# Optimization experiments

Hardware: AMD Instinct MI355X
Metric: run time of the kernel (lower is better)

Reference implementation:

```python
import jax, jax.numpy as jnp
import numpy as np

D_MODEL = 1024
N_HEADS = 16
K_TOP = 64
D_HEAD = D_MODEL // N_HEADS


def setup_inputs() -> dict:
    key = jax.random.key(0)
    ks = jax.random.split(key, 9)
    B, L = 8, 4096
    bound = 1.0 / np.sqrt(D_MODEL)  # nn.Linear default init range
    lin = lambda k: jax.random.uniform(k, (D_MODEL, D_MODEL), jnp.float32, -bound, bound)
    vec = lambda k: jax.random.uniform(k, (D_MODEL,), jnp.float32, -bound, bound)
    return {
        "query": jax.random.normal(ks[0], (B, L, D_MODEL), jnp.float32),
        "Wq": lin(ks[1]), "bq": vec(ks[2]),
        "Wk": lin(ks[3]), "bk": vec(ks[4]),
        "Wv": lin(ks[5]), "bv": vec(ks[6]),
        "Wo": lin(ks[7]), "bo": vec(ks[8]),
    }


def reference(query, Wq, bq, Wk, bk, Wv, bv, Wo, bo):
    B, L_q, D = query.shape
    L_k = L_q  # self-attention: key = value = query
    F_q = L_q // 2 + 1
    F_k = L_k // 2 + 1
    k_top = min(K_TOP, F_q)

    def proj(x, W, b):
        # (B, L, D) -> (B, H, L, d_head)
        return (x @ W + b).reshape(B, -1, N_HEADS, D_HEAD).transpose(0, 2, 1, 3)

    q = proj(query, Wq, bq)
    k = proj(query, Wk, bk)
    v = proj(query, Wv, bv)

    q_freq = jnp.fft.rfft(q, axis=2)  # (B, H, F_q, d_head) complex64
    k_freq = jnp.fft.rfft(k, axis=2)
    v_freq = jnp.fft.rfft(v, axis=2)

    # top-k frequency bins by mean spectral magnitude of the query
    q_energy = jnp.abs(q_freq).mean(axis=-1)  # (B, H, F_q)
    _, idx = jax.lax.top_k(q_energy, k_top)   # (B, H, k)
    mapped_idx = jnp.clip(
        jnp.round(idx.astype(jnp.float32) * (F_k - 1) / (F_q - 1)).astype(jnp.int32),
        0, F_k - 1)

    gather = lambda x, i: jnp.take_along_axis(x, i[..., None], axis=2)
    q_top = gather(q_freq, idx)          # (B, H, k, d_head)
    k_top_freq = gather(k_freq, mapped_idx)
    v_top = gather(v_freq, mapped_idx)

    eps = 1e-8
    attn_score = (q_top.real * k_top_freq.real).sum(-1) / (D_HEAD ** 0.5 + eps)
    attn = jax.nn.softmax(attn_score, axis=-1)[..., None]  # (B, H, k, 1)

    # fill spectrum with mean of query spectrum, then scatter attended bins
    q_mean_freq = q_freq.mean(axis=2, keepdims=True)  # (B, H, 1, d_head) complex
    out_freq = jnp.broadcast_to(q_mean_freq, (B, N_HEADS, F_q, D_HEAD))
    src = (attn * v_top.real).astype(out_freq.dtype)  # real -> complex (imag=0)
    bi = jnp.arange(B)[:, None, None]
    hi = jnp.arange(N_HEADS)[None, :, None]
    out_freq = out_freq.at[bi, hi, idx].set(src)

    out_time = jnp.fft.irfft(out_freq, n=L_q, axis=2)  # (B, H, L, d_head)
    out = out_time.transpose(0, 2, 1, 3).reshape(B, L_q, D)
    return out @ Wo + bo
```

## Files before the change

### kernel.cpp

```cpp
#include <hip/hip_runtime.h>
#include <math.h>
#include <stdint.h>


typedef _Float16 f16;
typedef _Float16 f16x4 __attribute__((ext_vector_type(4)));
typedef _Float16 f16x8 __attribute__((ext_vector_type(8)));
typedef float f32x4 __attribute__((ext_vector_type(4)));

#define PI_F 3.14159265358979323846f
#define PADJ(j) ((j) + ((j) >> 3))

__device__ __forceinline__ void gl_lds16(const void* g, void* l) {
  __builtin_amdgcn_global_load_lds((const __attribute__((address_space(1))) void*)g,
                                   (__attribute__((address_space(3))) void*)l, 16, 0, 0);
}

__device__ __forceinline__ float2 cadd(float2 a, float2 b) { return make_float2(a.x + b.x, a.y + b.y); }
__device__ __forceinline__ float2 csub(float2 a, float2 b) { return make_float2(a.x - b.x, a.y - b.y); }
__device__ __forceinline__ float2 cmul(float2 a, float2 b) {
  return make_float2(a.x * b.x - a.y * b.y, a.x * b.y + a.y * b.x);
}
__device__ __forceinline__ float2 cmni(float2 a) { return make_float2(a.y, -a.x); }

template <int NIT>
__device__ __forceinline__ void stgP(const char* g, size_t gstride, int kb, char* lds,
                                     int tid, int w) {
#pragma unroll
  for (int it = 0; it < NIT; ++it) {
    int ls = it * 256 + tid;
    int j = ls >> 3, s = ls & 7;
    int u = s ^ (j & 7);
    int grow = 2 * j + (u >> 2);
    gl_lds16(g + (size_t)grow * gstride + ((u & 3) << 4) + kb, lds + it * 4096 + w * 1024);
  }
}

__device__ __forceinline__ int pofs(int grow, int q) {
  int j = grow >> 1;
  int u = ((grow & 1) << 2) | q;
  return j * 128 + ((u ^ (j & 7)) << 4);
}

__global__ __launch_bounds__(256) void k_tw(float2* __restrict__ twtab, float2* __restrict__ utab) {
  int j = blockIdx.x * 256 + threadIdx.x;
  if (j < 2048) {
    float ang = (float)j * (-6.28318530717958647692f / 2048.0f);
    twtab[j] = make_float2(cosf(ang), sinf(ang));
  } else if (j < 4097) {
    int f = j - 2048;
    float ang = (float)f * (-6.28318530717958647692f / 4096.0f);
    utab[f] = make_float2(cosf(ang), sinf(ang));
  }
}

__global__ __launch_bounds__(256) void k_prep(const float* __restrict__ Wq, const float* __restrict__ Wo,
                                              f16* __restrict__ WqT, f16* __restrict__ WoT) {
  __shared__ float t[32][33];
  const float* src = blockIdx.z ? Wo : Wq;
  f16* dst = blockIdx.z ? WoT : WqT;
  int c0 = blockIdx.x * 32, r0 = blockIdx.y * 32;
  int tx = threadIdx.x, ty = threadIdx.y;
#pragma unroll
  for (int yy = 0; yy < 4; ++yy)
    t[ty + yy * 8][tx] = src[(size_t)(r0 + ty + yy * 8) * 1024 + c0 + tx];
  __syncthreads();
#pragma unroll
  for (int yy = 0; yy < 4; ++yy)
    dst[(size_t)(c0 + ty + yy * 8) * 1024 + r0 + tx] = (f16)t[tx][ty + yy * 8];
}

__global__ __launch_bounds__(256) void k_prep2(const float* __restrict__ Wk, const float* __restrict__ Wv,
                                               f16* __restrict__ WkT, f16* __restrict__ WvT) {
  __shared__ float t[32][33];
  const float* src = blockIdx.z ? Wv : Wk;
  f16* dst = blockIdx.z ? WvT : WkT;
  int c0 = blockIdx.x * 32, r0 = blockIdx.y * 32;
  int tx = threadIdx.x, ty = threadIdx.y;
#pragma unroll
  for (int yy = 0; yy < 4; ++yy)
    t[ty + yy * 8][tx] = src[(size_t)(r0 + ty + yy * 8) * 1024 + c0 + tx];
  __syncthreads();
#pragma unroll
  for (int yy = 0; yy < 4; ++yy)
    dst[(size_t)(c0 + ty + yy * 8) * 1024 + r0 + tx] = (f16)t[tx][ty + yy * 8];
}

__global__ __launch_bounds__(256) void k_t1(const float* __restrict__ X, f16* __restrict__ Xt16) {
  __shared__ float t[64][65];
  int b = blockIdx.z;
  int l0 = blockIdx.x * 64, d0 = blockIdx.y * 64;
  int tid = threadIdx.x;
#pragma unroll
  for (int it = 0; it < 16; ++it) {
    int lr = it * 4 + (tid >> 6);
    t[lr][tid & 63] = X[((size_t)b * 4096 + l0 + lr) * 1024 + d0 + (tid & 63)];
  }
  __syncthreads();
#pragma unroll
  for (int it = 0; it < 4; ++it) {
    int dd = it * 16 + (tid >> 4);
    int lc = (tid & 15) * 4;
    f16x4 v;
    v[0] = (f16)t[lc][dd]; v[1] = (f16)t[lc + 1][dd];
    v[2] = (f16)t[lc + 2][dd]; v[3] = (f16)t[lc + 3][dd];
    *(f16x4*)&Xt16[((size_t)b * 1024 + d0 + dd) * 4096 + l0 + lc] = v;
  }
}

__device__ __forceinline__ void r8_stage(const float2* __restrict__ cur, float2* __restrict__ nxt,
                                         const float2* __restrict__ tw, int tid, int lg) {
  int Ls = 1 << lg;
  int p = tid >> lg, q = tid & (Ls - 1);
  float2 x[8];
#pragma unroll
  for (int u = 0; u < 8; ++u) x[u] = cur[PADJ(tid + 256 * u)];
  float2 s0 = cadd(x[0], x[4]), d0v = csub(x[0], x[4]);
  float2 s1 = cadd(x[2], x[6]), d1v = csub(x[2], x[6]);
  float2 e0 = cadd(s0, s1), e2 = csub(s0, s1);
  float2 md1 = cmni(d1v);
  float2 e1 = cadd(d0v, md1), e3 = csub(d0v, md1);
  float2 t0 = cadd(x[1], x[5]), u0 = csub(x[1], x[5]);
  float2 t1 = cadd(x[3], x[7]), u1 = csub(x[3], x[7]);
  float2 o0 = cadd(t0, t1), o2 = csub(t0, t1);
  float2 mu1 = cmni(u1);
  float2 o1 = cadd(u0, mu1), o3 = csub(u0, mu1);
  const float C8 = 0.70710678118654752440f;
  float2 w1 = make_float2(C8 * (o1.x + o1.y), C8 * (o1.y - o1.x));
  float2 w2 = cmni(o2);
  float2 w3 = make_float2(C8 * (o3.y - o3.x), -C8 * (o3.x + o3.y));
  float2 y[8];
  y[0] = cadd(e0, o0); y[4] = csub(e0, o0);
  y[1] = cadd(e1, w1); y[5] = csub(e1, w1);
  y[2] = cadd(e2, w2); y[6] = csub(e2, w2);
  y[3] = cadd(e3, w3); y[7] = csub(e3, w3);
  int tb = p << lg;
#pragma unroll
  for (int v = 1; v < 8; ++v) y[v] = cmul(y[v], tw[tb * v]);
  int ob = q + (p << (lg + 3));
#pragma unroll
  for (int v = 0; v < 8; ++v) nxt[PADJ(ob + (v << lg))] = y[v];
}

__global__ __launch_bounds__(256) void k_fft(const f16* __restrict__ Xt16,
                                             const float2* __restrict__ twtab,
                                             const float2* __restrict__ utab,
                                             f16* __restrict__ PReU, f16* __restrict__ PImU,
                                             float* __restrict__ sumXf) {
  __shared__ float2 bufA[2304];
  __shared__ float2 bufB[2304];
  __shared__ float redr[256], redi[256];
  int tid = threadIdx.x;
  int blk = blockIdx.x;

  const f16x8* src = (const f16x8*)(Xt16 + (size_t)blk * 4096);
#pragma unroll
  for (int r = 0; r < 2; ++r) {
    int i8 = r * 256 + tid;
    f16x8 v = src[i8];
#pragma unroll
    for (int j = 0; j < 4; ++j)
      bufA[PADJ(4 * i8 + j)] = make_float2((float)v[2 * j], (float)v[2 * j + 1]);
  }
  __syncthreads();
  r8_stage(bufA, bufB, twtab, tid, 0);
  __syncthreads();
  r8_stage(bufB, bufA, twtab, tid, 3);
  __syncthreads();
  r8_stage(bufA, bufB, twtab, tid, 6);
  __syncthreads();
#pragma unroll
  for (int h = 0; h < 2; ++h) {
    int i = (h << 8) + tid;
    float2 a0 = bufB[PADJ(i)], a1 = bufB[PADJ(i + 512)];
    float2 a2 = bufB[PADJ(i + 1024)], a3 = bufB[PADJ(i + 1536)];
    float2 s02 = cadd(a0, a2), d02 = csub(a0, a2);
    float2 s13 = cadd(a1, a3), d13m = cmni(csub(a1, a3));
    bufA[PADJ(i)] = cadd(s02, s13);
    bufA[PADJ(i + 512)] = cadd(d02, d13m);
    bufA[PADJ(i + 1024)] = csub(s02, s13);
    bufA[PADJ(i + 1536)] = csub(d02, d13m);
  }
  __syncthreads();
  float sumr = 0.f, sumi = 0.f;
  size_t obase = (size_t)blk * 2049;
  for (int f = tid; f <= 2048; f += 256) {
    int fz = f & 2047, fm = (2048 - f) & 2047;
    float2 z = bufA[PADJ(fz)], m = bufA[PADJ(fm)];
    float Er = 0.5f * (z.x + m.x), Ei = 0.5f * (z.y - m.y);
    float Or = 0.5f * (z.y + m.y), Oi = -0.5f * (z.x - m.x);
    float2 wv = utab[f];
    float Xr = Er + wv.x * Or - wv.y * Oi;
    float Xi = Ei + wv.x * Oi + wv.y * Or;
    PReU[obase + f] = (f16)Xr;
    PImU[obase + f] = (f16)Xi;
    sumr += Xr; sumi += Xi;
  }
  __syncthreads();
  redr[tid] = sumr; redi[tid] = sumi;
  __syncthreads();
  for (int s = 128; s > 0; s >>= 1) {
    if (tid < s) { redr[tid] += redr[tid + s]; redi[tid] += redi[tid + s]; }
    __syncthreads();
  }
  if (tid == 0) { sumXf[2 * blk] = redr[0]; sumXf[2 * blk + 1] = redi[0]; }
}

__global__ __launch_bounds__(256) void k_C(const float* __restrict__ sumXf, const float* __restrict__ Wq,
                                           const float* __restrict__ bq,
                                           float* __restrict__ Cre, float* __restrict__ Cim) {
  int b = blockIdx.x >> 2;
  int hd = ((blockIdx.x & 3) << 8) + threadIdx.x;
  float accr = 0.f, acci = 0.f;
  for (int dm = 0; dm < 1024; ++dm) {
    float w = Wq[(size_t)dm * 1024 + hd];
    accr += sumXf[2 * (b * 1024 + dm)] * w;
    acci += sumXf[2 * (b * 1024 + dm) + 1] * w;
  }
  Cre[b * 1024 + hd] = (accr + 4096.0f * bq[hd]) * (1.0f / 2049.0f);
  Cim[b * 1024 + hd] = acci * (1.0f / 2049.0f);
}

__global__ __launch_bounds__(256) void k_t2(const f16* __restrict__ PReU, const f16* __restrict__ PImU,
                                            f16* __restrict__ PT) {
  __shared__ f16 t[32][66];
  int z = blockIdx.z;
  int b = z >> 1, pl = z & 1;
  const f16* src = pl ? PImU : PReU;
  int f0 = blockIdx.x * 32, d0 = blockIdx.y * 64;
  int tid = threadIdx.x;
#pragma unroll
  for (int p = 0; p < 8; ++p) {
    int dm = p * 8 + (tid >> 5);
    int ff = f0 + (tid & 31);
    t[tid & 31][dm] = (ff < 2049) ? src[(size_t)(b * 1024 + d0 + dm) * 2049 + ff] : (f16)0.f;
  }
  __syncthreads();
#pragma unroll
  for (int p = 0; p < 2; ++p) {
    int fr = p * 16 + (tid >> 4);
    int dm = (tid & 15) * 4;
    f16x4 v;
    v[0] = t[fr][dm]; v[1] = t[fr][dm + 1]; v[2] = t[fr][dm + 2]; v[3] = t[fr][dm + 3];
    *(f16x4*)&PT[((size_t)b * 4352 + 2 * (f0 + fr) + pl) * 1024 + d0 + dm] = v;
  }
}

__global__ __launch_bounds__(256, 2) void k_energy(const f16* __restrict__ PT, const f16* __restrict__ WqT,
                                                   const float* __restrict__ bq, float* __restrict__ energy) {
  __shared__ __align__(16) char sM[2][24576];
  int tid = threadIdx.x;
  int lane = tid & 63, w = tid >> 6;
  int lin = blockIdx.x;
  int sw = (lin & 7) * 136 + (lin >> 3);
  int bN = sw & 3, Mblk = sw >> 2;
  int wr = w >> 1, wc = w & 1;
  f32x4 acc[4][8];
#pragma unroll
  for (int mf = 0; mf < 4; ++mf)
#pragma unroll
    for (int nf = 0; nf < 8; ++nf) acc[mf][nf] = 0;

  const char* gA0 = (const char*)PT + (size_t)(Mblk * 128) * 2048;
  const char* gB0 = (const char*)WqT + (size_t)(bN * 256) * 2048;
  int r = lane & 15, q = lane >> 4;
  int aofs[4], bofs[8];
#pragma unroll
  for (int mf = 0; mf < 4; ++mf) aofs[mf] = pofs(wr * 64 + mf * 16 + r, q);
#pragma unroll
  for (int nf = 0; nf < 8; ++nf) bofs[nf] = 8192 + pofs(wc * 128 + nf * 16 + r, q);

  char* b0 = &sM[0][0];
  char* b1 = &sM[1][0];
  auto compute = [&](const char* base) {
    f16x8 aF[4], bF[8];
#pragma unroll
    for (int mf = 0; mf < 4; ++mf) aF[mf] = *(const f16x8*)(base + aofs[mf]);
#pragma unroll
    for (int nf = 0; nf < 8; ++nf) bF[nf] = *(const f16x8*)(base + bofs[nf]);
#pragma unroll
    for (int mf = 0; mf < 4; ++mf)
#pragma unroll
      for (int nf = 0; nf < 8; ++nf)
        acc[mf][nf] = __builtin_amdgcn_mfma_f32_16x16x32_f16(aF[mf], bF[nf], acc[mf][nf], 0, 0, 0);
  };

  stgP<2>(gA0, 2048, 0, b0, tid, w);
  stgP<4>(gB0, 2048, 0, b0 + 8192, tid, w);
  for (int t = 0; t < 16; ++t) {
    int kb1 = (2 * t + 1) * 64;
    stgP<2>(gA0, 2048, kb1, b1, tid, w);
    stgP<4>(gB0, 2048, kb1, b1 + 8192, tid, w);
    asm volatile("s_waitcnt vmcnt(6)\ns_barrier" ::: "memory");
    compute(b0);
    asm volatile("s_barrier" ::: "memory");
    if (t < 15) {
      int kb0 = (2 * t + 2) * 64;
      stgP<2>(gA0, 2048, kb0, b0, tid, w);
      stgP<4>(gB0, 2048, kb0, b0 + 8192, tid, w);
      asm volatile("s_waitcnt vmcnt(6)\ns_barrier" ::: "memory");
    } else {
      asm volatile("s_waitcnt vmcnt(0)\ns_barrier" ::: "memory");
    }
    compute(b1);
    asm volatile("s_barrier" ::: "memory");
  }
  int b = Mblk / 34;
  int tIb = Mblk - b * 34;
  int h0 = bN * 4 + wc * 2;
  bool dc0 = (tIb == 0 && wr == 0 && q == 0);
#pragma unroll
  for (int mf = 0; mf < 4; ++mf) {
    float sE0 = 0.f, sO0 = 0.f, sE1 = 0.f, sO1 = 0.f;
#pragma unroll
    for (int nf = 0; nf < 8; ++nf) {
      float re0 = acc[mf][nf][0], im0 = acc[mf][nf][1];
      float re1 = acc[mf][nf][2], im1 = acc[mf][nf][3];
      if (dc0 && mf == 0) re0 += 4096.0f * bq[(h0 + (nf >> 2)) * 64 + (nf & 3) * 16 + r];
      float m0 = sqrtf(re0 * re0 + im0 * im0);
      float m1 = sqrtf(re1 * re1 + im1 * im1);
      if (nf < 4) { sE0 += m0; sO0 += m1; } else { sE1 += m0; sO1 += m1; }
    }
#pragma unroll
    for (int off = 1; off < 16; off <<= 1) {
      sE0 += __shfl_xor(sE0, off);
      sO0 += __shfl_xor(sO0, off);
      sE1 += __shfl_xor(sE1, off);
      sO1 += __shfl_xor(sO1, off);
    }
    if (r == 0) {
      int fp = tIb * 64 + wr * 32 + mf * 8 + (q << 1);
      energy[((size_t)b * 16 + h0) * 2176 + fp] = sE0 * 0.015625f;
      energy[((size_t)b * 16 + h0) * 2176 + fp + 1] = sO0 * 0.015625f;
      energy[((size_t)b * 16 + h0 + 1) * 2176 + fp] = sE1 * 0.015625f;
      energy[((size_t)b * 16 + h0 + 1) * 2176 + fp + 1] = sO1 * 0.015625f;
    }
  }
}

__global__ __launch_bounds__(256) void k_topk(const float* __restrict__ energy, int* __restrict__ idxb) {
  __shared__ float vals[2049];
  __shared__ unsigned long long wbest[4];
  int tid = threadIdx.x, bh = blockIdx.x;
  const float* e = energy + (size_t)bh * 2176;
  for (int i = tid; i < 2049; i += 256) vals[i] = e[i];
  __syncthreads();
  for (int it = 0; it < 64; ++it) {
    unsigned long long best = 0ull;
    for (int f = tid; f < 2049; f += 256) {
      unsigned b32 = __float_as_uint(vals[f]);
      b32 = (b32 & 0x80000000u) ? ~b32 : (b32 | 0x80000000u);
      unsigned long long k = ((unsigned long long)b32 << 12) | (unsigned)(4095 - f);
      best = (k > best) ? k : best;
    }
#pragma unroll
    for (int off = 32; off > 0; off >>= 1) {
      unsigned long long o = __shfl_xor(best, off);
      best = (o > best) ? o : best;
    }
    if ((tid & 63) == 0) wbest[tid >> 6] = best;
    __syncthreads();
    if (tid == 0) {
      unsigned long long b0 = wbest[0] > wbest[1] ? wbest[0] : wbest[1];
      unsigned long long b1 = wbest[2] > wbest[3] ? wbest[2] : wbest[3];
      unsigned long long bb = b0 > b1 ? b0 : b1;
      int f = 4095 - (int)(bb & 4095ull);
      idxb[bh * 64 + it] = f;
      vals[f] = -1.0f;
    }
    __syncthreads();
  }
}

__global__ __launch_bounds__(256) void k_qkv(const f16* __restrict__ PT, const int* __restrict__ idxb,
                                             const f16* __restrict__ WqT, const f16* __restrict__ WkT,
                                             const f16* __restrict__ WvT, float* __restrict__ part) {
  __shared__ __align__(16) f16 sA[64 * 64];
  __shared__ __align__(16) f16 sB[192 * 64];
  __shared__ int fjs[64];
  int tid = threadIdx.x, lane = tid & 63, w = tid >> 6;
  int bh = blockIdx.x, ks = blockIdx.y;
  int b = bh >> 4, h = bh & 15;
  if (tid < 64) fjs[tid] = idxb[bh * 64 + tid];
  __syncthreads();
  f32x4 acc[4][3];
#pragma unroll
  for (int mf = 0; mf < 4; ++mf)
#pragma unroll
    for (int nf = 0; nf < 3; ++nf) acc[mf][nf] = 0;

  int l8 = lane & 7;
  int lr = lane >> 3;
  int swz = (l8 ^ lr) << 4;

  for (int kt = 0; kt < 4; ++kt) {
    int kbyte = ks * 512 + kt * 128;
#pragma unroll
    for (int t = 0; t < 2; ++t) {
      int ia = w * 2 + t;
      int row = ia * 8 + lr;
      const char* src = (const char*)PT + (size_t)(b * 4352 + 2 * fjs[row]) * 2048 + kbyte + swz;
      gl_lds16(src, (char*)sA + ia * 1024);
    }
#pragma unroll
    for (int t = 0; t < 6; ++t) {
      int ib = w * 6 + t;
      int row = ib * 8 + lr;
      const f16* Wt = (row < 64) ? WqT : (row < 128) ? WkT : WvT;
      const char* src = (const char*)Wt + (size_t)(h * 64 + (row & 63)) * 2048 + kbyte + swz;
      gl_lds16(src, (char*)sB + ib * 1024);
    }
    __syncthreads();
#pragma unroll
    for (int kk = 0; kk < 64; kk += 32) {
      int cb = (kk << 1) + ((lane >> 4) << 4);
      int r = lane & 15;
      f16x8 aF[4], bF[3];
#pragma unroll
      for (int mf = 0; mf < 4; ++mf) {
        int row = mf * 16 + r;
        aF[mf] = *(const f16x8*)((const char*)sA + row * 128 + (cb ^ ((row & 7) << 4)));
      }
#pragma unroll
      for (int nf = 0; nf < 3; ++nf) {
        int row = w * 48 + nf * 16 + r;
        bF[nf] = *(const f16x8*)((const char*)sB + row * 128 + (cb ^ ((row & 7) << 4)));
      }
#pragma unroll
      for (int mf = 0; mf < 4; ++mf)
#pragma unroll
        for (int nf = 0; nf < 3; ++nf)
          acc[mf][nf] = __builtin_amdgcn_mfma_f32_16x16x32_f16(aF[mf], bF[nf], acc[mf][nf], 0, 0, 0);
    }
    __syncthreads();
  }
  float* pb = part + (size_t)(ks * 128 + bh) * 12288;
#pragma unroll
  for (int mf = 0; mf < 4; ++mf)
#pragma unroll
    for (int nf = 0; nf < 3; ++nf)
#pragma unroll
      for (int rr = 0; rr < 4; ++rr) {
        int m = mf * 16 + ((lane >> 4) << 2) + rr;
        int n = w * 48 + nf * 16 + (lane & 15);
        pb[m * 192 + n] = acc[mf][nf][rr];
      }
}

__global__ __launch_bounds__(256) void k_attn2(const float* __restrict__ part, const int* __restrict__ idxb,
                                               const float* __restrict__ bq, const float* __restrict__ bk,
                                               const float* __restrict__ bv, const float* __restrict__ Cre,
                                               f16* __restrict__ ampT) {
  __shared__ float sQKV[64][196];
  __shared__ float scores[64], attns[64];
  __shared__ int fjs[64];
  __shared__ int dcrow;
  int tid = threadIdx.x, bh = blockIdx.x;
  int b = bh >> 4, h = bh & 15;
  if (tid == 0) dcrow = -1;
  __syncthreads();
  if (tid < 64) {
    int f = idxb[bh * 64 + tid];
    fjs[tid] = f;
    if (f == 0) dcrow = tid;
  }
  __syncthreads();
  const float4* p0 = (const float4*)(part + (size_t)bh * 12288);
  const size_t s4 = (size_t)128 * 12288 / 4;
#pragma unroll
  for (int it = 0; it < 12; ++it) {
    int e = it * 256 + tid;
    float4 v0 = p0[e], v1 = p0[e + s4], v2 = p0[e + 2 * s4], v3 = p0[e + 3 * s4];
    float4 v;
    v.x = v0.x + v1.x + v2.x + v3.x;
    v.y = v0.y + v1.y + v2.y + v3.y;
    v.z = v0.z + v1.z + v2.z + v3.z;
    v.w = v0.w + v1.w + v2.w + v3.w;
    int m = e / 48, n0 = (e % 48) * 4;
    *(float4*)&sQKV[m][n0] = v;
  }
  __syncthreads();
  if (dcrow >= 0 && tid < 192) {
    const float* bias = (tid < 64) ? bq : (tid < 128) ? bk : bv;
    sQKV[dcrow][tid] += 4096.0f * bias[h * 64 + (tid & 63)];
  }
  __syncthreads();
  {
    int j = tid >> 2, p = tid & 3;
    float s = 0.f;
#pragma unroll
    for (int c = 0; c < 16; ++c) {
      int cc = p * 16 + c;
      s = fmaf(sQKV[j][cc], sQKV[j][64 + cc], s);
    }
    s += __shfl_xor(s, 1);
    s += __shfl_xor(s, 2);
    if (p == 0) scores[j] = s * 0.125f;
  }
  __syncthreads();
  if (tid < 64) {
    float s = scores[tid];
    float m = s;
#pragma unroll
    for (int off = 32; off > 0; off >>= 1) m = fmaxf(m, __shfl_xor(m, off));
    float ev = expf(s - m);
    float sm = ev;
#pragma unroll
    for (int off = 32; off > 0; off >>= 1) sm += __shfl_xor(sm, off);
    attns[tid] = ev / sm;
  }
  __syncthreads();
  {
    int j = tid >> 2, d0 = (tid & 3) * 16;
    float at = attns[j];
    int fj = fjs[j];
    float wj = (fj == 0 || fj == 2048) ? 0.5f : 1.0f;
#pragma unroll
    for (int q4 = 0; q4 < 4; ++q4) {
      float4 c4 = *(const float4*)&Cre[b * 1024 + h * 64 + d0 + q4 * 4];
      float4 vv = *(const float4*)&sQKV[j][128 + d0 + q4 * 4];
      float av0 = wj * (at * vv.x - c4.x);
      float av1 = wj * (at * vv.y - c4.y);
      float av2 = wj * (at * vv.z - c4.z);
      float av3 = wj * (at * vv.w - c4.w);
      f16* o = ampT + (size_t)bh * 4096 + (d0 + q4 * 4) * 64 + j;
      o[0] = (f16)av0; o[64] = (f16)av1; o[128] = (f16)av2; o[192] = (f16)av3;
    }
  }
}

__global__ __launch_bounds__(256) void k_ot(const f16* __restrict__ ampT, const int* __restrict__ idxb,
                                            const float* __restrict__ Cre, const float* __restrict__ Cim,
                                            f16* __restrict__ OT) {
  __shared__ __align__(16) f16 sAmp[64][72];
  __shared__ float gbuf[256];
  __shared__ int fjs[64];
  int tid = threadIdx.x, lane = tid & 63, w = tid >> 6;
  int bh = blockIdx.x >> 4, tch = blockIdx.x & 15;
  int b = bh >> 4, h = bh & 15;
  if (tid < 64) fjs[tid] = idxb[bh * 64 + tid];
  {
    int row = tid >> 2, seg = tid & 3;
    const f16* src = ampT + (size_t)bh * 4096 + row * 64 + seg * 16;
    f16x8 v0 = *(const f16x8*)src;
    f16x8 v1 = *(const f16x8*)(src + 8);
    *(f16x8*)&sAmp[row][seg * 16] = v0;
    *(f16x8*)&sAmp[row][seg * 16 + 8] = v1;
  }
  __syncthreads();
  int r = lane & 15, q = lane >> 4;
  int tbase = tch * 256 + w * 64;
  const float cang = 0.00153398078788564123f;
  f16x8 aF[4][2];
  float ss[4];
#pragma unroll
  for (int mf = 0; mf < 4; ++mf) {
    int t = tbase + mf * 16 + r;
    float s = 0.f;
#pragma unroll
    for (int kk2 = 0; kk2 < 2; ++kk2) {
      f16x8 a;
#pragma unroll
      for (int jj = 0; jj < 8; ++jj) {
        int j = kk2 * 32 + q * 8 + jj;
        int ridx = (fjs[j] * t) & 4095;
        float sn, cs;
        __sincosf((float)ridx * cang, &sn, &cs);
        s += sn;
        a[jj] = (f16)cs;
      }
      aF[mf][kk2] = a;
    }
    ss[mf] = s;
  }
#pragma unroll
  for (int mf = 0; mf < 4; ++mf) {
    ss[mf] += __shfl_xor(ss[mf], 16);
    ss[mf] += __shfl_xor(ss[mf], 32);
  }
  if (q == 0) {
#pragma unroll
    for (int mf = 0; mf < 4; ++mf) {
      int t = tbase + mf * 16 + r;
      float g = ss[mf];
      if (t & 1) {
        int tp = (t <= 2048) ? t : 4096 - t;
        float sg = (t <= 2048) ? 1.f : -1.f;
        float aa = (float)tp * (PI_F / 4096.0f);
        g -= sg * (cosf(aa) / sinf(aa));
      }
      gbuf[w * 64 + mf * 16 + r] = g;
    }
  }
  f16x8 bF[4][2];
#pragma unroll
  for (int nf = 0; nf < 4; ++nf)
#pragma unroll
    for (int kk2 = 0; kk2 < 2; ++kk2)
      bF[nf][kk2] = *(const f16x8*)&sAmp[nf * 16 + r][kk2 * 32 + q * 8];
  f32x4 acc[4][4];
#pragma unroll
  for (int mf = 0; mf < 4; ++mf)
#pragma unroll
    for (int nf = 0; nf < 4; ++nf) acc[mf][nf] = 0;
#pragma unroll
  for (int kk2 = 0; kk2 < 2; ++kk2)
#pragma unroll
    for (int mf = 0; mf < 4; ++mf)
#pragma unroll
      for (int nf = 0; nf < 4; ++nf)
        acc[mf][nf] = __builtin_amdgcn_mfma_f32_16x16x32_f16(aF[mf][kk2], bF[nf][kk2], acc[mf][nf], 0, 0, 0);
  __syncthreads();
  const float s2L = 2.0f / 4096.0f;
#pragma unroll
  for (int nf = 0; nf < 4; ++nf) {
    int d = nf * 16 + r;
    float cim = Cim[b * 1024 + h * 64 + d];
    float cre = Cre[b * 1024 + h * 64 + d];
#pragma unroll
    for (int mf = 0; mf < 4; ++mf) {
#pragma unroll
      for (int rr = 0; rr < 4; ++rr) {
        int ro = mf * 16 + q * 4 + rr;
        int t = tbase + ro;
        float g = gbuf[w * 64 + ro];
        float val = s2L * (acc[mf][nf][rr] + cim * g) + ((t == 0) ? cre : 0.f);
        OT[((size_t)bh * 4096 + t) * 64 + d] = (f16)val;
      }
    }
  }
}

__global__ __launch_bounds__(256, 2) void k_final(const f16* __restrict__ OT, const f16* __restrict__ WoT,
                                                  const float* __restrict__ bo, float* __restrict__ out) {
  __shared__ __align__(16) char sM[2][24576];
  int tid = threadIdx.x, lane = tid & 63, w = tid >> 6;
  int lin = blockIdx.x;
  int sw = (lin & 7) * 128 + (lin >> 3);
  int bN = sw & 3, Mblk = sw >> 2;
  int wr = w >> 1, wc = w & 1;
  f32x4 acc[4][8];
#pragma unroll
  for (int mf = 0; mf < 4; ++mf)
#pragma unroll
    for (int nf = 0; nf < 8; ++nf) acc[mf][nf] = 0;
  int b = Mblk >> 5, t0 = (Mblk & 31) * 128;
  const char* gB0 = (const char*)WoT + (size_t)(bN * 256) * 2048;
  int r = lane & 15, q = lane >> 4;
  int aofs[4], bofs[8];
#pragma unroll
  for (int mf = 0; mf < 4; ++mf) aofs[mf] = pofs(wr * 64 + mf * 16 + r, q);
#pragma unroll
  for (int nf = 0; nf < 8; ++nf) bofs[nf] = 8192 + pofs(wc * 128 + nf * 16 + r, q);
#define GA_HEAD(ks) ((const char*)OT + ((size_t)(b * 16 + ((ks) >> 1)) * 4096 + t0) * 128)

  char* b0 = &sM[0][0];
  char* b1 = &sM[1][0];
  auto compute = [&](const char* base) {
    f16x8 aF[4], bF[8];
#pragma unroll
    for (int mf = 0; mf < 4; ++mf) aF[mf] = *(const f16x8*)(base + aofs[mf]);
#pragma unroll
    for (int nf = 0; nf < 8; ++nf) bF[nf] = *(const f16x8*)(base + bofs[nf]);
#pragma unroll
    for (int mf = 0; mf < 4; ++mf)
#pragma unroll
      for (int nf = 0; nf < 8; ++nf)
        acc[mf][nf] = __builtin_amdgcn_mfma_f32_16x16x32_f16(aF[mf], bF[nf], acc[mf][nf], 0, 0, 0);
  };

  stgP<2>(GA_HEAD(0), 128, 0, b0, tid, w);
  stgP<4>(gB0, 2048, 0, b0 + 8192, tid, w);
  for (int t = 0; t < 16; ++t) {
    int ks1 = 2 * t + 1;
    stgP<2>(GA_HEAD(ks1), 128, (ks1 & 1) * 64, b1, tid, w);
    stgP<4>(gB0, 2048, ks1 * 64, b1 + 8192, tid, w);
    asm volatile("s_waitcnt vmcnt(6)\ns_barrier" ::: "memory");
    compute(b0);
    asm volatile("s_barrier" ::: "memory");
    if (t < 15) {
      int ks0 = 2 * t + 2;
      stgP<2>(GA_HEAD(ks0), 128, (ks0 & 1) * 64, b0, tid, w);
      stgP<4>(gB0, 2048, ks0 * 64, b0 + 8192, tid, w);
      asm volatile("s_waitcnt vmcnt(6)\ns_barrier" ::: "memory");
    } else {
      asm volatile("s_waitcnt vmcnt(0)\ns_barrier" ::: "memory");
    }
    compute(b1);
    asm volatile("s_barrier" ::: "memory");
  }
#undef GA_HEAD
#pragma unroll
  for (int nf = 0; nf < 8; ++nf) {
    int gcol = bN * 256 + wc * 128 + nf * 16 + r;
    float bcol = bo[gcol];
#pragma unroll
    for (int mf = 0; mf < 4; ++mf) {
#pragma unroll
      for (int rr = 0; rr < 4; ++rr) {
        int grow = Mblk * 128 + wr * 64 + mf * 16 + (q << 2) + rr;
        out[(size_t)grow * 1024 + gcol] = acc[mf][nf][rr] + bcol;
      }
    }
  }
}

extern "C" void kernel_launch(void* const* d_in, const int* in_sizes, int n_in,
                              void* d_out, int out_size, void* d_ws, size_t ws_size,
                              hipStream_t stream) {
  const float* X = (const float*)d_in[0];
  const float* Wq = (const float*)d_in[1];
  const float* bq = (const float*)d_in[2];
  const float* Wk = (const float*)d_in[3];
  const float* bk = (const float*)d_in[4];
  const float* Wv = (const float*)d_in[5];
  const float* bv = (const float*)d_in[6];
  const float* Wo = (const float*)d_in[7];
  const float* bo = (const float*)d_in[8];
  float* out = (float*)d_out;

  if (ws_size < 208928768ULL) return;
  char* w = (char*)d_ws;
  f16* Xt16 = (f16*)(w);
  f16* PT = (f16*)(w);
  f16* WkT = (f16*)(w + 71303168);
  f16* WvT = (f16*)(w + 73400320);
  float* part = (float*)(w + 75497472);
  char* R2 = w + 134217728;
  f16* PReU = (f16*)(R2);
  f16* PImU = (f16*)(R2 + 33570816);
  f16* OT = (f16*)(R2);
  char* R3 = R2 + 67141632;
  float* sumXf = (float*)(R3);
  float* Cre = (float*)(R3 + 65536);
  float* Cim = (float*)(R3 + 98304);
  float* energy = (float*)(R3 + 131072);
  int* idxb = (int*)(R3 + 1245184);
  f16* ampT = (f16*)(R3 + 1277952);
  f16* WqT = (f16*)(R3 + 3375104);
  f16* WoT = (f16*)(R3 + 5472256);
  float2* twtab = (float2*)d_out;
  float2* utab = twtab + 2048;

  dim3 b32(32, 8);
  hipLaunchKernelGGL(k_tw, dim3(17), dim3(256), 0, stream, twtab, utab);
  hipLaunchKernelGGL(k_prep, dim3(32, 32, 2), b32, 0, stream, Wq, Wo, WqT, WoT);
  hipLaunchKernelGGL(k_t1, dim3(64, 16, 8), dim3(256), 0, stream, X, Xt16);
  hipLaunchKernelGGL(k_fft, dim3(8192), dim3(256), 0, stream, Xt16, twtab, utab, PReU, PImU, sumXf);
  hipLaunchKernelGGL(k_prep2, dim3(32, 32, 2), b32, 0, stream, Wk, Wv, WkT, WvT);
  hipLaunchKernelGGL(k_C, dim3(32), dim3(256), 0, stream, sumXf, Wq, bq, Cre, Cim);
  hipLaunchKernelGGL(k_t2, dim3(68, 16, 16), dim3(256), 0, stream, PReU, PImU, PT);
  hipLaunchKernelGGL(k_energy, dim3(1088), dim3(256), 0, stream, PT, WqT, bq, energy);
  hipLaunchKernelGGL(k_topk, dim3(128), dim3(256), 0, stream, energy, idxb);
  hipLaunchKernelGGL(k_qkv, dim3(128, 4), dim3(256), 0, stream, PT, idxb, WqT, WkT, WvT, part);
  hipLaunchKernelGGL(k_attn2, dim3(128), dim3(256), 0, stream, part, idxb, bq, bk, bv, Cre, ampT);
  hipLaunchKernelGGL(k_ot, dim3(2048), dim3(256), 0, stream, ampT, idxb, Cre, Cim, OT);
  hipLaunchKernelGGL(k_final, dim3(1024), dim3(256), 0, stream, OT, WoT, bo, out);
}
```

Baseline: 474.0 us.

## Enlarge k_energy tile to 256x256 using 32x32x16 MFMA

The energy GEMM now uses 256x256 output tiles per block instead of 128x256, halving the grid to 544 blocks. It switches from 16x16x32 to 32x32x16 MFMA instructions and rewrites the epilogue reduction for the new accumulator layout. The aim is more reuse of each loaded LDS byte and fewer fragment loads per MFMA. In exchange it needs more LDS and registers, so only one block fits per CU, and the smaller grid may leave CUs underused.

Result: slower. 516.0 us (+8.9%).

```diff
diff --git a/kernel.cpp b/kernel.cpp
--- a/kernel.cpp
+++ b/kernel.cpp
@@ -7,6 +7,7 @@
 typedef _Float16 f16x4 __attribute__((ext_vector_type(4)));
 typedef _Float16 f16x8 __attribute__((ext_vector_type(8)));
 typedef float f32x4 __attribute__((ext_vector_type(4)));
+typedef float f32x16 __attribute__((ext_vector_type(16)));
 
 #define PI_F 3.14159265358979323846f
 #define PADJ(j) ((j) + ((j) >> 3))
@@ -246,94 +247,109 @@
   }
 }
 
-__global__ __launch_bounds__(256, 2) void k_energy(const f16* __restrict__ PT, const f16* __restrict__ WqT,
+__global__ __launch_bounds__(256, 1) void k_energy(const f16* __restrict__ PT, const f16* __restrict__ WqT,
                                                    const float* __restrict__ bq, float* __restrict__ energy) {
-  __shared__ __align__(16) char sM[2][24576];
+  __shared__ __align__(16) char sM[2][32768];
   int tid = threadIdx.x;
   int lane = tid & 63, w = tid >> 6;
   int lin = blockIdx.x;
-  int sw = (lin & 7) * 136 + (lin >> 3);
+  int sw = (lin & 7) * 68 + (lin >> 3);
   int bN = sw & 3, Mblk = sw >> 2;
   int wr = w >> 1, wc = w & 1;
-  f32x4 acc[4][8];
+  int l31 = lane & 31, l5 = lane >> 5;
+  f32x16 acc[4][4];
 #pragma unroll
   for (int mf = 0; mf < 4; ++mf)
 #pragma unroll
-    for (int nf = 0; nf < 8; ++nf) acc[mf][nf] = 0;
-
-  const char* gA0 = (const char*)PT + (size_t)(Mblk * 128) * 2048;
+    for (int nf = 0; nf < 4; ++nf) acc[mf][nf] = 0;
+
+  const char* gA0 = (const char*)PT + (size_t)(Mblk * 256) * 2048;
   const char* gB0 = (const char*)WqT + (size_t)(bN * 256) * 2048;
-  int r = lane & 15, q = lane >> 4;
-  int aofs[4], bofs[8];
-#pragma unroll
-  for (int mf = 0; mf < 4; ++mf) aofs[mf] = pofs(wr * 64 + mf * 16 + r, q);
-#pragma unroll
-  for (int nf = 0; nf < 8; ++nf) bofs[nf] = 8192 + pofs(wc * 128 + nf * 16 + r, q);
+  int aofs[4][2], bofs[4][2];
+#pragma unroll
+  for (int mf = 0; mf < 4; ++mf)
+#pragma unroll
+    for (int ks2 = 0; ks2 < 2; ++ks2)
+      aofs[mf][ks2] = pofs(wr * 128 + mf * 32 + l31, ks2 * 2 + l5);
+#pragma unroll
+  for (int nf = 0; nf < 4; ++nf)
+#pragma unroll
+    for (int ks2 = 0; ks2 < 2; ++ks2)
+      bofs[nf][ks2] = 16384 + pofs(wc * 128 + nf * 32 + l31, ks2 * 2 + l5);
 
   char* b0 = &sM[0][0];
   char* b1 = &sM[1][0];
+  auto stage = [&](int ks, char* buf) {
+    stgP<4>(gA0, 2048, ks * 64, buf, tid, w);
+    stgP<4>(gB0, 2048, ks * 64, buf + 16384, tid, w);
+  };
   auto compute = [&](const char* base) {
-    f16x8 aF[4], bF[8];
-#pragma unroll
-    for (int mf = 0; mf < 4; ++mf) aF[mf] = *(const f16x8*)(base + aofs[mf]);
-#pragma unroll
-    for (int nf = 0; nf < 8; ++nf) bF[nf] = *(const f16x8*)(base + bofs[nf]);
+    f16x8 aF[4][2], bF[4][2];
 #pragma unroll
     for (int mf = 0; mf < 4; ++mf)
 #pragma unroll
-      for (int nf = 0; nf < 8; ++nf)
-        acc[mf][nf] = __builtin_amdgcn_mfma_f32_16x16x32_f16(aF[mf], bF[nf], acc[mf][nf], 0, 0, 0);
+      for (int ks2 = 0; ks2 < 2; ++ks2) aF[mf][ks2] = *(const f16x8*)(base + aofs[mf][ks2]);
+#pragma unroll
+    for (int nf = 0; nf < 4; ++nf)
+#pragma unroll
+      for (int ks2 = 0; ks2 < 2; ++ks2) bF[nf][ks2] = *(const f16x8*)(base + bofs[nf][ks2]);
+#pragma unroll
+    for (int ks2 = 0; ks2 < 2; ++ks2)
+#pragma unroll
+      for (int mf = 0; mf < 4; ++mf)
+#pragma unroll
+        for (int nf = 0; nf < 4; ++nf)
+          acc[mf][nf] = __builtin_amdgcn_mfma_f32_32x32x16_f16(aF[mf][ks2], bF[nf][ks2], acc[mf][nf], 0, 0, 0);
   };
 
-  stgP<2>(gA0, 2048, 0, b0, tid, w);
-  stgP<4>(gB0, 2048, 0, b0 + 8192, tid, w);
+  stage(0, b0);
   for (int t = 0; t < 16; ++t) {
-    int kb1 = (2 * t + 1) * 64;
-    stgP<2>(gA0, 2048, kb1, b1, tid, w);
-    stgP<4>(gB0, 2048, kb1, b1 + 8192, tid, w);
-    asm volatile("s_waitcnt vmcnt(6)\ns_barrier" ::: "memory");
+    stage(2 * t + 1, b1);
+    asm volatile("s_waitcnt vmcnt(8)\ns_barrier" ::: "memory");
     compute(b0);
     asm volatile("s_barrier" ::: "memory");
     if (t < 15) {
-      int kb0 = (2 * t + 2) * 64;
-      stgP<2>(gA0, 2048, kb0, b0, tid, w);
-      stgP<4>(gB0, 2048, kb0, b0 + 8192, tid, w);
-      asm volatile("s_waitcnt vmcnt(6)\ns_barrier" ::: "memory");
+      stage(2 * t + 2, b0);
+      asm volatile("s_waitcnt vmcnt(8)\ns_barrier" ::: "memory");
     } else {
       asm volatile("s_waitcnt vmcnt(0)\ns_barrier" ::: "memory");
     }
     compute(b1);
     asm volatile("s_barrier" ::: "memory");
   }
-  int b = Mblk / 34;
-  int tIb = Mblk - b * 34;
-  int h0 = bN * 4 + wc * 2;
-  bool dc0 = (tIb == 0 && wr == 0 && q == 0);
+  int b = Mblk / 17;
+  int tIb = Mblk - b * 17;
+  bool dc = (tIb == 0 && wr == 0 && l5 == 0);
 #pragma unroll
   for (int mf = 0; mf < 4; ++mf) {
-    float sE0 = 0.f, sO0 = 0.f, sE1 = 0.f, sO1 = 0.f;
-#pragma unroll
-    for (int nf = 0; nf < 8; ++nf) {
-      float re0 = acc[mf][nf][0], im0 = acc[mf][nf][1];
-      float re1 = acc[mf][nf][2], im1 = acc[mf][nf][3];
-      if (dc0 && mf == 0) re0 += 4096.0f * bq[(h0 + (nf >> 2)) * 64 + (nf & 3) * 16 + r];
-      float m0 = sqrtf(re0 * re0 + im0 * im0);
-      float m1 = sqrtf(re1 * re1 + im1 * im1);
-      if (nf < 4) { sE0 += m0; sO0 += m1; } else { sE1 += m0; sO1 += m1; }
-    }
-#pragma unroll
-    for (int off = 1; off < 16; off <<= 1) {
-      sE0 += __shfl_xor(sE0, off);
-      sO0 += __shfl_xor(sO0, off);
-      sE1 += __shfl_xor(sE1, off);
-      sO1 += __shfl_xor(sO1, off);
-    }
-    if (r == 0) {
-      int fp = tIb * 64 + wr * 32 + mf * 8 + (q << 1);
-      energy[((size_t)b * 16 + h0) * 2176 + fp] = sE0 * 0.015625f;
-      energy[((size_t)b * 16 + h0) * 2176 + fp + 1] = sO0 * 0.015625f;
-      energy[((size_t)b * 16 + h0 + 1) * 2176 + fp] = sE1 * 0.015625f;
-      energy[((size_t)b * 16 + h0 + 1) * 2176 + fp + 1] = sO1 * 0.015625f;
+#pragma unroll
+    for (int hh = 0; hh < 2; ++hh) {
+      int head = bN * 4 + wc * 2 + hh;
+      float ms[8];
+#pragma unroll
+      for (int p = 0; p < 8; ++p) {
+        float s = 0.f;
+#pragma unroll
+        for (int half = 0; half < 2; ++half) {
+          int nf = hh * 2 + half;
+          float re = acc[mf][nf][2 * p];
+          float im = acc[mf][nf][2 * p + 1];
+          if (dc && mf == 0 && p == 0) re += 4096.0f * bq[head * 64 + half * 32 + l31];
+          s += sqrtf(re * re + im * im);
+        }
+        ms[p] = s;
+      }
+#pragma unroll
+      for (int off = 1; off < 32; off <<= 1)
+#pragma unroll
+        for (int p = 0; p < 8; ++p) ms[p] += __shfl_xor(ms[p], off);
+      if (l31 == 0) {
+#pragma unroll
+        for (int p = 0; p < 8; ++p) {
+          int fp = tIb * 128 + wr * 64 + mf * 16 + ((p & 1) + 4 * (p >> 1) + 2 * l5);
+          energy[((size_t)b * 16 + head) * 2176 + fp] = ms[p] * 0.015625f;
+        }
+      }
     }
   }
 }
@@ -750,7 +766,7 @@
   hipLaunchKernelGGL(k_prep2, dim3(32, 32, 2), b32, 0, stream, Wk, Wv, WkT, WvT);
   hipLaunchKernelGGL(k_C, dim3(32), dim3(256), 0, stream, sumXf, Wq, bq, Cre, Cim);
   hipLaunchKernelGGL(k_t2, dim3(68, 16, 16), dim3(256), 0, stream, PReU, PImU, PT);
-  hipLaunchKernelGGL(k_energy, dim3(1088), dim3(256), 0, stream, PT, WqT, bq, energy);
+  hipLaunchKernelGGL(k_energy, dim3(544), dim3(256), 0, stream, PT, WqT, bq, energy);
   hipLaunchKernelGGL(k_topk, dim3(128), dim3(256), 0, stream, energy, idxb);
   hipLaunchKernelGGL(k_qkv, dim3(128, 4), dim3(256), 0, stream, PT, idxb, WqT, WkT, WvT, part);
   hipLaunchKernelGGL(k_attn2, dim3(128), dim3(256), 0, stream, part, idxb, bq, bk, bv, Cre, ampT);
```

## Enlarge energy and final GEMM tiles to 256x256 with 8-wave blocks

Applied to the files above, without the earlier changes.

The energy and output-projection GEMMs move from 128x256 tiles with 4 waves to 256x256 tiles with 8 waves (512 threads, one block per CU), and the grid is halved. Each step now stages A and B with an inline swizzled global-to-LDS load split into two halves, interleaved with half-compute phases. The aim is more operand reuse per byte loaded and fewer blocks. The cost is one block per CU with fewer blocks overall, which can hurt latency hiding and leave CUs unevenly loaded, plus full vmcnt(0) waits each step.

Result: slower. 501.9 us (+5.9%).

```diff
diff --git a/kernel.cpp b/kernel.cpp
--- a/kernel.cpp
+++ b/kernel.cpp
@@ -246,94 +246,99 @@
   }
 }
 
-__global__ __launch_bounds__(256, 2) void k_energy(const f16* __restrict__ PT, const f16* __restrict__ WqT,
+__global__ __launch_bounds__(512, 1) void k_energy(const f16* __restrict__ PT, const f16* __restrict__ WqT,
                                                    const float* __restrict__ bq, float* __restrict__ energy) {
-  __shared__ __align__(16) char sM[2][24576];
+  __shared__ __align__(16) char sM[2][32768];
   int tid = threadIdx.x;
   int lane = tid & 63, w = tid >> 6;
   int lin = blockIdx.x;
-  int sw = (lin & 7) * 136 + (lin >> 3);
+  int sw = (lin & 7) * 68 + (lin >> 3);
   int bN = sw & 3, Mblk = sw >> 2;
-  int wr = w >> 1, wc = w & 1;
-  f32x4 acc[4][8];
-#pragma unroll
-  for (int mf = 0; mf < 4; ++mf)
-#pragma unroll
-    for (int nf = 0; nf < 8; ++nf) acc[mf][nf] = 0;
-
-  const char* gA0 = (const char*)PT + (size_t)(Mblk * 128) * 2048;
+  int wr = w >> 2, wc = w & 3;
+  f32x4 acc[8][4];
+#pragma unroll
+  for (int mf = 0; mf < 8; ++mf)
+#pragma unroll
+    for (int nf = 0; nf < 4; ++nf) acc[mf][nf] = 0;
+
+  const char* gA0 = (const char*)PT + (size_t)(Mblk * 256) * 2048;
   const char* gB0 = (const char*)WqT + (size_t)(bN * 256) * 2048;
   int r = lane & 15, q = lane >> 4;
-  int aofs[4], bofs[8];
-#pragma unroll
-  for (int mf = 0; mf < 4; ++mf) aofs[mf] = pofs(wr * 64 + mf * 16 + r, q);
-#pragma unroll
-  for (int nf = 0; nf < 8; ++nf) bofs[nf] = 8192 + pofs(wc * 128 + nf * 16 + r, q);
+  int aofs[8], bofs[4];
+#pragma unroll
+  for (int mf = 0; mf < 8; ++mf) aofs[mf] = pofs(wr * 128 + mf * 16 + r, q);
+#pragma unroll
+  for (int nf = 0; nf < 4; ++nf) bofs[nf] = 16384 + pofs(wc * 64 + nf * 16 + r, q);
 
   char* b0 = &sM[0][0];
   char* b1 = &sM[1][0];
-  auto compute = [&](const char* base) {
-    f16x8 aF[4], bF[8];
-#pragma unroll
-    for (int mf = 0; mf < 4; ++mf) aF[mf] = *(const f16x8*)(base + aofs[mf]);
-#pragma unroll
-    for (int nf = 0; nf < 8; ++nf) bF[nf] = *(const f16x8*)(base + bofs[nf]);
-#pragma unroll
-    for (int mf = 0; mf < 4; ++mf)
-#pragma unroll
-      for (int nf = 0; nf < 8; ++nf)
-        acc[mf][nf] = __builtin_amdgcn_mfma_f32_16x16x32_f16(aF[mf], bF[nf], acc[mf][nf], 0, 0, 0);
+  auto stg = [&](const char* g, int kb, char* dst, int it) {
+    int ls = it * 512 + tid;
+    int j = ls >> 3, s = ls & 7;
+    int u = s ^ (j & 7);
+    int grow = 2 * j + (u >> 2);
+    gl_lds16(g + (size_t)grow * 2048 + ((u & 3) << 4) + kb, dst + it * 8192 + w * 1024);
   };
-
-  stgP<2>(gA0, 2048, 0, b0, tid, w);
-  stgP<4>(gB0, 2048, 0, b0 + 8192, tid, w);
-  for (int t = 0; t < 16; ++t) {
-    int kb1 = (2 * t + 1) * 64;
-    stgP<2>(gA0, 2048, kb1, b1, tid, w);
-    stgP<4>(gB0, 2048, kb1, b1 + 8192, tid, w);
-    asm volatile("s_waitcnt vmcnt(6)\ns_barrier" ::: "memory");
-    compute(b0);
+  auto computeH = [&](const char* base, int mh) {
+    f16x8 aF[4], bF[4];
+#pragma unroll
+    for (int i = 0; i < 4; ++i) aF[i] = *(const f16x8*)(base + aofs[mh * 4 + i]);
+#pragma unroll
+    for (int nf = 0; nf < 4; ++nf) bF[nf] = *(const f16x8*)(base + bofs[nf]);
+#pragma unroll
+    for (int i = 0; i < 4; ++i)
+#pragma unroll
+      for (int nf = 0; nf < 4; ++nf)
+        acc[mh * 4 + i][nf] = __builtin_amdgcn_mfma_f32_16x16x32_f16(aF[i], bF[nf], acc[mh * 4 + i][nf], 0, 0, 0);
+  };
+
+  stg(gA0, 0, b0, 0); stg(gA0, 0, b0, 1);
+  stg(gB0, 0, b0 + 16384, 0); stg(gB0, 0, b0 + 16384, 1);
+  asm volatile("s_waitcnt vmcnt(0)\ns_barrier" ::: "memory");
+  for (int t2 = 0; t2 < 16; ++t2) {
+    int kb1 = (2 * t2 + 1) * 64;
+    stg(gA0, kb1, b1, 0); stg(gA0, kb1, b1, 1);
+    computeH(b0, 0);
     asm volatile("s_barrier" ::: "memory");
-    if (t < 15) {
-      int kb0 = (2 * t + 2) * 64;
-      stgP<2>(gA0, 2048, kb0, b0, tid, w);
-      stgP<4>(gB0, 2048, kb0, b0 + 8192, tid, w);
-      asm volatile("s_waitcnt vmcnt(6)\ns_barrier" ::: "memory");
+    stg(gB0, kb1, b1 + 16384, 0); stg(gB0, kb1, b1 + 16384, 1);
+    computeH(b0, 1);
+    asm volatile("s_waitcnt vmcnt(0)\ns_barrier" ::: "memory");
+    if (t2 < 15) {
+      int kb0 = (2 * t2 + 2) * 64;
+      stg(gA0, kb0, b0, 0); stg(gA0, kb0, b0, 1);
+      computeH(b1, 0);
+      asm volatile("s_barrier" ::: "memory");
+      stg(gB0, kb0, b0 + 16384, 0); stg(gB0, kb0, b0 + 16384, 1);
+      computeH(b1, 1);
+      asm volatile("s_waitcnt vmcnt(0)\ns_barrier" ::: "memory");
     } else {
-      asm volatile("s_waitcnt vmcnt(0)\ns_barrier" ::: "memory");
-    }
-    compute(b1);
-    asm volatile("s_barrier" ::: "memory");
-  }
-  int b = Mblk / 34;
-  int tIb = Mblk - b * 34;
-  int h0 = bN * 4 + wc * 2;
-  bool dc0 = (tIb == 0 && wr == 0 && q == 0);
-#pragma unroll
-  for (int mf = 0; mf < 4; ++mf) {
-    float sE0 = 0.f, sO0 = 0.f, sE1 = 0.f, sO1 = 0.f;
-#pragma unroll
-    for (int nf = 0; nf < 8; ++nf) {
+      computeH(b1, 0);
+      computeH(b1, 1);
+    }
+  }
+  int b = Mblk / 17, tIb = Mblk - b * 17;
+  int head = bN * 4 + wc;
+  bool dc = (tIb == 0 && wr == 0 && q == 0);
+#pragma unroll
+  for (int mf = 0; mf < 8; ++mf) {
+    float sE = 0.f, sO = 0.f;
+#pragma unroll
+    for (int nf = 0; nf < 4; ++nf) {
       float re0 = acc[mf][nf][0], im0 = acc[mf][nf][1];
       float re1 = acc[mf][nf][2], im1 = acc[mf][nf][3];
-      if (dc0 && mf == 0) re0 += 4096.0f * bq[(h0 + (nf >> 2)) * 64 + (nf & 3) * 16 + r];
-      float m0 = sqrtf(re0 * re0 + im0 * im0);
-      float m1 = sqrtf(re1 * re1 + im1 * im1);
-      if (nf < 4) { sE0 += m0; sO0 += m1; } else { sE1 += m0; sO1 += m1; }
+      if (dc && mf == 0) re0 += 4096.0f * bq[head * 64 + nf * 16 + r];
+      sE += sqrtf(re0 * re0 + im0 * im0);
+      sO += sqrtf(re1 * re1 + im1 * im1);
     }
 #pragma unroll
     for (int off = 1; off < 16; off <<= 1) {
-      sE0 += __shfl_xor(sE0, off);
-      sO0 += __shfl_xor(sO0, off);
-      sE1 += __shfl_xor(sE1, off);
-      sO1 += __shfl_xor(sO1, off);
+      sE += __shfl_xor(sE, off);
+      sO += __shfl_xor(sO, off);
     }
     if (r == 0) {
-      int fp = tIb * 64 + wr * 32 + mf * 8 + (q << 1);
-      energy[((size_t)b * 16 + h0) * 2176 + fp] = sE0 * 0.015625f;
-      energy[((size_t)b * 16 + h0) * 2176 + fp + 1] = sO0 * 0.015625f;
-      energy[((size_t)b * 16 + h0 + 1) * 2176 + fp] = sE1 * 0.015625f;
-      energy[((size_t)b * 16 + h0 + 1) * 2176 + fp + 1] = sO1 * 0.015625f;
+      int fp = tIb * 128 + wr * 64 + mf * 8 + (q << 1);
+      energy[((size_t)b * 16 + head) * 2176 + fp] = sE * 0.015625f;
+      energy[((size_t)b * 16 + head) * 2176 + fp + 1] = sO * 0.015625f;
     }
   }
 }
@@ -631,74 +636,93 @@
   }
 }
 
-__global__ __launch_bounds__(256, 2) void k_final(const f16* __restrict__ OT, const f16* __restrict__ WoT,
+__global__ __launch_bounds__(512, 1) void k_final(const f16* __restrict__ OT, const f16* __restrict__ WoT,
                                                   const float* __restrict__ bo, float* __restrict__ out) {
-  __shared__ __align__(16) char sM[2][24576];
-  int tid = threadIdx.x, lane = tid & 63, w = tid >> 6;
+  __shared__ __align__(16) char sM[2][32768];
+  int tid = threadIdx.x;
+  int lane = tid & 63, w = tid >> 6;
   int lin = blockIdx.x;
-  int sw = (lin & 7) * 128 + (lin >> 3);
+  int sw = (lin & 7) * 64 + (lin >> 3);
   int bN = sw & 3, Mblk = sw >> 2;
-  int wr = w >> 1, wc = w & 1;
-  f32x4 acc[4][8];
-#pragma unroll
-  for (int mf = 0; mf < 4; ++mf)
-#pragma unroll
-    for (int nf = 0; nf < 8; ++nf) acc[mf][nf] = 0;
-  int b = Mblk >> 5, t0 = (Mblk & 31) * 128;
+  int wr = w >> 2, wc = w & 3;
+  f32x4 acc[8][4];
+#pragma unroll
+  for (int mf = 0; mf < 8; ++mf)
+#pragma unroll
+    for (int nf = 0; nf < 4; ++nf) acc[mf][nf] = 0;
+  int b = Mblk >> 4, t0 = (Mblk & 15) * 256;
   const char* gB0 = (const char*)WoT + (size_t)(bN * 256) * 2048;
   int r = lane & 15, q = lane >> 4;
-  int aofs[4], bofs[8];
-#pragma unroll
-  for (int mf = 0; mf < 4; ++mf) aofs[mf] = pofs(wr * 64 + mf * 16 + r, q);
-#pragma unroll
-  for (int nf = 0; nf < 8; ++nf) bofs[nf] = 8192 + pofs(wc * 128 + nf * 16 + r, q);
-#define GA_HEAD(ks) ((const char*)OT + ((size_t)(b * 16 + ((ks) >> 1)) * 4096 + t0) * 128)
+  int aofs[8], bofs[4];
+#pragma unroll
+  for (int mf = 0; mf < 8; ++mf) aofs[mf] = pofs(wr * 128 + mf * 16 + r, q);
+#pragma unroll
+  for (int nf = 0; nf < 4; ++nf) bofs[nf] = 16384 + pofs(wc * 64 + nf * 16 + r, q);
 
   char* b0 = &sM[0][0];
   char* b1 = &sM[1][0];
-  auto compute = [&](const char* base) {
-    f16x8 aF[4], bF[8];
-#pragma unroll
-    for (int mf = 0; mf < 4; ++mf) aF[mf] = *(const f16x8*)(base + aofs[mf]);
-#pragma unroll
-    for (int nf = 0; nf < 8; ++nf) bF[nf] = *(const f16x8*)(base + bofs[nf]);
-#pragma unroll
-    for (int mf = 0; mf < 4; ++mf)
-#pragma unroll
-      for (int nf = 0; nf < 8; ++nf)
-        acc[mf][nf] = __builtin_amdgcn_mfma_f32_16x16x32_f16(aF[mf], bF[nf], acc[mf][nf], 0, 0, 0);
+  auto stgA = [&](int ks, char* dst, int it) {
+    const char* g = (const char*)OT + ((size_t)(b * 16 + (ks >> 1)) * 4096 + t0) * 128;
+    int kb = (ks & 1) * 64;
+    int ls = it * 512 + tid;
+    int j = ls >> 3, s = ls & 7;
+    int u = s ^ (j & 7);
+    int grow = 2 * j + (u >> 2);
+    gl_lds16(g + (size_t)grow * 128 + ((u & 3) << 4) + kb, dst + it * 8192 + w * 1024);
   };
-
-  stgP<2>(GA_HEAD(0), 128, 0, b0, tid, w);
-  stgP<4>(gB0, 2048, 0, b0 + 8192, tid, w);
-  for (int t = 0; t < 16; ++t) {
-    int ks1 = 2 * t + 1;
-    stgP<2>(GA_HEAD(ks1), 128, (ks1 & 1) * 64, b1, tid, w);
-    stgP<4>(gB0, 2048, ks1 * 64, b1 + 8192, tid, w);
-    asm volatile("s_waitcnt vmcnt(6)\ns_barrier" ::: "memory");
-    compute(b0);
+  auto stgB = [&](int ks, char* dst, int it) {
+    int ls = it * 512 + tid;
+    int j = ls >> 3, s = ls & 7;
+    int u = s ^ (j & 7);
+    int grow = 2 * j + (u >> 2);
+    gl_lds16(gB0 + (size_t)grow * 2048 + ((u & 3) << 4) + ks * 64, dst + it * 8192 + w * 1024);
+  };
+  auto computeH = [&](const char* base, int mh) {
+    f16x8 aF[4], bF[4];
+#pragma unroll
+    for (int i = 0; i < 4; ++i) aF[i] = *(const f16x8*)(base + aofs[mh * 4 + i]);
+#pragma unroll
+    for (int nf = 0; nf < 4; ++nf) bF[nf] = *(const f16x8*)(base + bofs[nf]);
+#pragma unroll
+    for (int i = 0; i < 4; ++i)
+#pragma unroll
+      for (int nf = 0; nf < 4; ++nf)
+        acc[mh * 4 + i][nf] = __builtin_amdgcn_mfma_f32_16x16x32_f16(aF[i], bF[nf], acc[mh * 4 + i][nf], 0, 0, 0);
+  };
+
+  stgA(0, b0, 0); stgA(0, b0, 1);
+  stgB(0, b0 + 16384, 0); stgB(0, b0 + 16384, 1);
+  asm volatile("s_waitcnt vmcnt(0)\ns_barrier" ::: "memory");
+  for (int t2 = 0; t2 < 16; ++t2) {
+    int ks1 = 2 * t2 + 1;
+    stgA(ks1, b1, 0); stgA(ks1, b1, 1);
+    computeH(b0, 0);
     asm volatile("s_barrier" ::: "memory");
-    if (t < 15) {
-      int ks0 = 2 * t + 2;
-      stgP<2>(GA_HEAD(ks0), 128, (ks0 & 1) * 64, b0, tid, w);
-      stgP<4>(gB0, 2048, ks0 * 64, b0 + 8192, tid, w);
-      asm volatile("s_waitcnt vmcnt(6)\ns_barrier" ::: "memory");
+    stgB(ks1, b1 + 16384, 0); stgB(ks1, b1 + 16384, 1);
+    computeH(b0, 1);
+    asm volatile("s_waitcnt vmcnt(0)\ns_barrier" ::: "memory");
+    if (t2 < 15) {
+      int ks0 = 2 * t2 + 2;
+      stgA(ks0, b0, 0); stgA(ks0, b0, 1);
+      computeH(b1, 0);
+      asm volatile("s_barrier" ::: "memory");
+      stgB(ks0, b0 + 16384, 0); stgB(ks0, b0 + 16384, 1);
+      computeH(b1, 1);
+      asm volatile("s_waitcnt vmcnt(0)\ns_barrier" ::: "memory");
     } else {
-      asm volatile("s_waitcnt vmcnt(0)\ns_barrier" ::: "memory");
-    }
-    compute(b1);
-    asm volatile("s_barrier" ::: "memory");
-  }
-#undef GA_HEAD
-#pragma unroll
-  for (int nf = 0; nf < 8; ++nf) {
-    int gcol = bN * 256 + wc * 128 + nf * 16 + r;
+      computeH(b1, 0);
+      computeH(b1, 1);
+    }
+  }
+#pragma unroll
+  for (int nf = 0; nf < 4; ++nf) {
+    int gcol = bN * 256 + wc * 64 + nf * 16 + r;
     float bcol = bo[gcol];
 #pragma unroll
-    for (int mf = 0; mf < 4; ++mf) {
+    for (int mf = 0; mf < 8; ++mf) {
 #pragma unroll
       for (int rr = 0; rr < 4; ++rr) {
-        int grow = Mblk * 128 + wr * 64 + mf * 16 + (q << 2) + rr;
+        int grow = Mblk * 256 + wr * 128 + mf * 16 + (q << 2) + rr;
         out[(size_t)grow * 1024 + gcol] = acc[mf][nf][rr] + bcol;
       }
     }
@@ -750,10 +774,10 @@
   hipLaunchKernelGGL(k_prep2, dim3(32, 32, 2), b32, 0, stream, Wk, Wv, WkT, WvT);
   hipLaunchKernelGGL(k_C, dim3(32), dim3(256), 0, stream, sumXf, Wq, bq, Cre, Cim);
   hipLaunchKernelGGL(k_t2, dim3(68, 16, 16), dim3(256), 0, stream, PReU, PImU, PT);
-  hipLaunchKernelGGL(k_energy, dim3(1088), dim3(256), 0, stream, PT, WqT, bq, energy);
+  hipLaunchKernelGGL(k_energy, dim3(544), dim3(512), 0, stream, PT, WqT, bq, energy);
   hipLaunchKernelGGL(k_topk, dim3(128), dim3(256), 0, stream, energy, idxb);
   hipLaunchKernelGGL(k_qkv, dim3(128, 4), dim3(256), 0, stream, PT, idxb, WqT, WkT, WvT, part);
   hipLaunchKernelGGL(k_attn2, dim3(128), dim3(256), 0, stream, part, idxb, bq, bk, bv, Cre, ampT);
   hipLaunchKernelGGL(k_ot, dim3(2048), dim3(256), 0, stream, ampT, idxb, Cre, Cim, OT);
-  hipLaunchKernelGGL(k_final, dim3(1024), dim3(256), 0, stream, OT, WoT, bo, out);
-}
+  hipLaunchKernelGGL(k_final, dim3(512), dim3(512), 0, stream, OT, WoT, bo, out);
+}
```
